# Kernel tuning notes

Measured on AMD Instinct MI355X. Metric: run time of the kernel, lower is better.

Reference implementation:

```python
import jax, jax.numpy as jnp
import numpy as np

D, H, DOUT, E, B = 1024, 4096, 1024, 8, 8192
TOP_K = 2


def setup_inputs() -> dict:
    key = jax.random.key(0)
    ks = jax.random.split(key, 12)
    s = 0.02
    return {
        "x": jax.random.normal(ks[0], (B, D), jnp.float32),
        # stacked expert params: Linear(D,H) -> ReLU -> Linear(H,H//2) -> ReLU -> Linear(H//2,DOUT)
        "W1": jax.random.normal(ks[1], (E, D, H), jnp.float32) * s,
        "b1": jnp.zeros((E, H), jnp.float32),
        "W2": jax.random.normal(ks[2], (E, H, H // 2), jnp.float32) * s,
        "b2": jnp.zeros((E, H // 2), jnp.float32),
        "W3": jax.random.normal(ks[3], (E, H // 2, DOUT), jnp.float32) * s,
        "b3": jnp.zeros((E, DOUT), jnp.float32),
        # gate: Linear(D, D//2) -> ReLU -> Linear(D//2, E) -> Softmax
        "Wg1": jax.random.normal(ks[4], (D, D // 2), jnp.float32) * s,
        "bg1": jnp.zeros((D // 2,), jnp.float32),
        "Wg2": jax.random.normal(ks[5], (D // 2, E), jnp.float32) * s,
        "bg2": jnp.zeros((E,), jnp.float32),
    }


def reference(x, W1, b1, W2, b2, W3, b3, Wg1, bg1, Wg2, bg2):
    # inference-mode math: dropout identity, no gate noise (training=False)
    num_experts = W1.shape[0]
    # gate weights: softmax over experts, [B, E]
    g = jax.nn.relu(x @ Wg1 + bg1)
    gate_weights = jax.nn.softmax(g @ Wg2 + bg2, axis=-1)
    # top-k routing, renormalized with softmax over selected logits
    top_w, top_idx = jax.lax.top_k(gate_weights, TOP_K)  # [B, k]
    top_w = jax.nn.softmax(top_w, axis=-1)
    # dense all-expert MLPs (as the original does): [E, B, *]
    h1 = jax.nn.relu(jnp.einsum("bd,edh->ebh", x, W1) + b1[:, None, :])
    h2 = jax.nn.relu(jnp.einsum("ebh,ehm->ebm", h1, W2) + b2[:, None, :])
    eo = jnp.einsum("ebm,emo->ebo", h2, W3) + b3[:, None, :]  # [E, B, DOUT]
    eo = jnp.swapaxes(eo, 0, 1)  # [B, E, DOUT]
    # gather top-k expert outputs and combine
    sel = jnp.take_along_axis(eo, top_idx[:, :, None], axis=1)  # [B, k, DOUT]
    final_output = jnp.sum(top_w[:, :, None] * sel, axis=1)  # [B, DOUT]
    # load balance loss on the (pre-topk) gate distribution
    expert_usage = jnp.mean(gate_weights, axis=0)
    load_balance_loss = jnp.mean((expert_usage - 1.0 / num_experts) ** 2)
    return final_output, load_balance_loss
```

## Files before the change

### kernel.cpp

```cpp
#include <hip/hip_runtime.h>

#define B_ROWS 8192
#define DDIM 1024
#define HDIM 4096
#define H2DIM 2048
#define DOUT_N 1024
#define NEXP 8
#define ROW_TILES 136
#define PAD_ROWS (ROW_TILES*128)

typedef __attribute__((ext_vector_type(8))) short short8;
typedef __attribute__((ext_vector_type(4))) float f32x4;

__device__ inline unsigned short f2bf(float f) {
  unsigned int u = __builtin_bit_cast(unsigned int, f);
  u += 0x7fffu + ((u >> 16) & 1u);
  return (unsigned short)(u >> 16);
}

__device__ inline void gld_lds16(const void* g, void* l) {
  __builtin_amdgcn_global_load_lds(
      (const __attribute__((address_space(1))) void*)g,
      (__attribute__((address_space(3))) void*)l, 16, 0, 0);
}

__global__ __launch_bounds__(256) void gate1_kernel(
    const float* __restrict__ x, const float* __restrict__ Wg1,
    const float* __restrict__ bg1, float* __restrict__ g) {
  __shared__ float a_s[16][132];
  __shared__ float b_s[16][64];
  const int t = threadIdx.x;
  const int row0 = blockIdx.y * 128;
  const int n0 = blockIdx.x * 64;
  const int tx = t & 15, ty = t >> 4;
  float c[8][4] = {};
  const int la_row = t >> 2, la_kq = (t & 3) * 4;
  const int lb_kk = t >> 4, lb_c = (t & 15) * 4;
  for (int k0 = 0; k0 < DDIM; k0 += 16) {
#pragma unroll
    for (int i = 0; i < 2; ++i) {
      int row = la_row + i * 64;
      float4 av = *(const float4*)&x[(size_t)(row0 + row) * DDIM + k0 + la_kq];
      a_s[la_kq + 0][row] = av.x; a_s[la_kq + 1][row] = av.y;
      a_s[la_kq + 2][row] = av.z; a_s[la_kq + 3][row] = av.w;
    }
    *(float4*)&b_s[lb_kk][lb_c] = *(const float4*)&Wg1[(size_t)(k0 + lb_kk) * 512 + n0 + lb_c];
    __syncthreads();
#pragma unroll
    for (int kk = 0; kk < 16; ++kk) {
      float4 b4 = *(const float4*)&b_s[kk][tx * 4];
      float4 a4lo = *(const float4*)&a_s[kk][ty * 8];
      float4 a4hi = *(const float4*)&a_s[kk][ty * 8 + 4];
      float aa[8] = {a4lo.x, a4lo.y, a4lo.z, a4lo.w, a4hi.x, a4hi.y, a4hi.z, a4hi.w};
      float bb[4] = {b4.x, b4.y, b4.z, b4.w};
#pragma unroll
      for (int i = 0; i < 8; ++i)
#pragma unroll
        for (int j = 0; j < 4; ++j) c[i][j] += aa[i] * bb[j];
    }
    __syncthreads();
  }
  float bb[4];
#pragma unroll
  for (int j = 0; j < 4; ++j) bb[j] = bg1[n0 + tx * 4 + j];
#pragma unroll
  for (int i = 0; i < 8; ++i) {
    float4 v;
    v.x = fmaxf(c[i][0] + bb[0], 0.f);
    v.y = fmaxf(c[i][1] + bb[1], 0.f);
    v.z = fmaxf(c[i][2] + bb[2], 0.f);
    v.w = fmaxf(c[i][3] + bb[3], 0.f);
    *(float4*)&g[(size_t)(row0 + ty * 8 + i) * 512 + n0 + tx * 4] = v;
  }
}

__global__ __launch_bounds__(256) void gate2_kernel(
    const float* __restrict__ g, const float* __restrict__ Wg2,
    const float* __restrict__ bg2, int* __restrict__ top_idx,
    float* __restrict__ top_w, int* __restrict__ counts,
    float* __restrict__ usage) {
  __shared__ float w2t[NEXP * 512];
  __shared__ float us[NEXP];
  __shared__ int cs[NEXP];
  const int t = threadIdx.x;
  for (int i = t; i < NEXP * 512; i += 256) {
    int k = i >> 3, e = i & 7;
    w2t[e * 512 + k] = Wg2[i];
  }
  if (t < NEXP) { us[t] = 0.f; cs[t] = 0; }
  __syncthreads();
  const int lane = t & 63, wid = t >> 6;
  const int row = blockIdx.x * 4 + wid;
  float part[NEXP] = {};
  const float* grow = &g[(size_t)row * 512];
#pragma unroll
  for (int j = 0; j < 8; ++j) {
    int k = lane + j * 64;
    float gv = grow[k];
#pragma unroll
    for (int e = 0; e < NEXP; ++e) part[e] += gv * w2t[e * 512 + k];
  }
#pragma unroll
  for (int e = 0; e < NEXP; ++e)
    for (int m = 32; m >= 1; m >>= 1) part[e] += __shfl_xor(part[e], m);
  if (lane == 0) {
    float p[NEXP];
    float mx = -1e30f;
#pragma unroll
    for (int e = 0; e < NEXP; ++e) { p[e] = part[e] + bg2[e]; mx = fmaxf(mx, p[e]); }
    float s = 0.f;
#pragma unroll
    for (int e = 0; e < NEXP; ++e) { p[e] = expf(p[e] - mx); s += p[e]; }
    float inv = 1.f / s;
#pragma unroll
    for (int e = 0; e < NEXP; ++e) { p[e] *= inv; atomicAdd(&us[e], p[e]); }
    int i0 = 0; float b0 = p[0];
    for (int e = 1; e < NEXP; ++e) if (p[e] > b0) { b0 = p[e]; i0 = e; }
    int i1 = -1; float b1 = -1.f;
    for (int e = 0; e < NEXP; ++e) {
      if (e == i0) continue;
      if (p[e] > b1) { b1 = p[e]; i1 = e; }
    }
    float e1 = expf(b1 - b0);
    float w0 = 1.f / (1.f + e1);
    top_idx[row * 2 + 0] = i0; top_idx[row * 2 + 1] = i1;
    top_w[row * 2 + 0] = w0;   top_w[row * 2 + 1] = e1 * w0;
    atomicAdd(&cs[i0], 1); atomicAdd(&cs[i1], 1);
  }
  __syncthreads();
  if (t < NEXP) { atomicAdd(&usage[t], us[t]); atomicAdd(&counts[t], cs[t]); }
}

__global__ void offsets_kernel(const int* __restrict__ counts, int* __restrict__ off) {
  if (threadIdx.x == 0) {
    int acc = 0;
    off[0] = 0;
    for (int e = 0; e < NEXP; ++e) {
      acc += (counts[e] + 127) & ~127;
      off[e + 1] = acc;
    }
  }
}

__global__ __launch_bounds__(256) void scatter_kernel(
    const int* __restrict__ top_idx, const int* __restrict__ off,
    int* __restrict__ fill, int* __restrict__ entry) {
  int row = blockIdx.x * 256 + threadIdx.x;
#pragma unroll
  for (int k = 0; k < 2; ++k) {
    int e = top_idx[row * 2 + k];
    int pos = atomicAdd(&fill[e], 1);
    entry[off[e] + pos] = row * 2 + k;
  }
}

__global__ __launch_bounds__(256) void gather_kernel(
    const float* __restrict__ x, const int* __restrict__ entry,
    unsigned short* __restrict__ Xg) {
  const int r = blockIdx.x;
  const int s = entry[r];
  const int t = threadIdx.x;
  unsigned long long packed = 0ull;
  if (s >= 0) {
    float4 f = *(const float4*)&x[(size_t)(s >> 1) * DDIM + t * 4];
    packed = (unsigned long long)f2bf(f.x) |
             ((unsigned long long)f2bf(f.y) << 16) |
             ((unsigned long long)f2bf(f.z) << 32) |
             ((unsigned long long)f2bf(f.w) << 48);
  }
  *(unsigned long long*)&Xg[(size_t)r * DDIM + t * 4] = packed;
}

__global__ __launch_bounds__(256) void transpose_kernel(
    const float* __restrict__ src, unsigned short* __restrict__ dst,
    int K, int N) {
  __shared__ float tile[64][65];
  const size_t eoff = (size_t)blockIdx.z * K * N;
  const int k0 = blockIdx.y * 64, n0 = blockIdx.x * 64;
  const int t = threadIdx.x;
#pragma unroll
  for (int i = 0; i < 16; ++i) {
    int idx = t + i * 256;
    int kk = idx >> 6, nn = idx & 63;
    tile[kk][nn] = src[eoff + (size_t)(k0 + kk) * N + n0 + nn];
  }
  __syncthreads();
#pragma unroll
  for (int i = 0; i < 16; ++i) {
    int idx = t + i * 256;
    int nn = idx >> 6, kk = idx & 63;
    dst[eoff + (size_t)(n0 + nn) * K + k0 + kk] = f2bf(tile[kk][nn]);
  }
}

template <int KDIM, int EPI>
__global__ __launch_bounds__(256) void expert_gemm(
    const unsigned short* __restrict__ A, const unsigned short* __restrict__ Bt,
    const float* __restrict__ bias, unsigned short* __restrict__ Cout,
    float* __restrict__ dOut, const float* __restrict__ topw,
    const int* __restrict__ entry, const int* __restrict__ off, int N) {
  const int tileM = blockIdx.y * 128;
  if (tileM >= off[NEXP]) return;
  int e = 0;
  while (e < NEXP - 1 && off[e + 1] <= tileM) ++e;
  const int tileN = blockIdx.x * 128;
  __shared__ unsigned short a_s[128 * 32];
  __shared__ unsigned short b_s[128 * 32];
  const int t = threadIdx.x;
  const int lane = t & 63, wid = t >> 6;
  const int wr = (wid & 1) * 64, wc = (wid >> 1) * 64;
  const int l16 = lane & 15, q = lane >> 4;
  f32x4 acc[4][4];
#pragma unroll
  for (int i = 0; i < 4; ++i)
#pragma unroll
    for (int j = 0; j < 4; ++j) acc[i][j] = (f32x4){0.f, 0.f, 0.f, 0.f};
  const unsigned short* Abase = A + (size_t)tileM * KDIM;
  const unsigned short* Bbase = Bt + ((size_t)e * N + tileN) * (size_t)KDIM;
  const int srow = 32 * wid;
  const int lrow = lane >> 2;
  const int lch = (lane & 3) * 8;
  for (int k0 = 0; k0 < KDIM; k0 += 32) {
#pragma unroll
    for (int j = 0; j < 2; ++j) {
      const int r0 = srow + 16 * j;
      gld_lds16(Abase + (size_t)(r0 + lrow) * KDIM + k0 + lch, &a_s[r0 * 32]);
      gld_lds16(Bbase + (size_t)(r0 + lrow) * KDIM + k0 + lch, &b_s[r0 * 32]);
    }
    __syncthreads();
    short8 af[4], bf[4];
#pragma unroll
    for (int i = 0; i < 4; ++i) {
      af[i] = *(const short8*)&a_s[(wr + 16 * i + l16) * 32 + q * 8];
      bf[i] = *(const short8*)&b_s[(wc + 16 * i + l16) * 32 + q * 8];
    }
#pragma unroll
    for (int i = 0; i < 4; ++i)
#pragma unroll
      for (int j = 0; j < 4; ++j)
        acc[i][j] = __builtin_amdgcn_mfma_f32_16x16x32_bf16(af[i], bf[j], acc[i][j], 0, 0, 0);
    __syncthreads();
  }
  if (EPI == 0) {
#pragma unroll
    for (int j = 0; j < 4; ++j) {
      const int gCol = tileN + wc + 16 * j + l16;
      const float bcol = bias[e * N + gCol];
#pragma unroll
      for (int i = 0; i < 4; ++i)
#pragma unroll
        for (int r = 0; r < 4; ++r) {
          const int gRow = tileM + wr + 16 * i + q * 4 + r;
          Cout[(size_t)gRow * N + gCol] = f2bf(fmaxf(acc[i][j][r] + bcol, 0.f));
        }
    }
  } else {
    float bcol[4];
#pragma unroll
    for (int j = 0; j < 4; ++j) bcol[j] = bias[e * N + tileN + wc + 16 * j + l16];
#pragma unroll
    for (int i = 0; i < 4; ++i)
#pragma unroll
      for (int r = 0; r < 4; ++r) {
        const int gRow = tileM + wr + 16 * i + q * 4 + r;
        const int s = entry[gRow];
        if (s < 0) continue;
        const float w = topw[s];
        float* orow = dOut + (size_t)(s >> 1) * N;
#pragma unroll
        for (int j = 0; j < 4; ++j) {
          const int gCol = tileN + wc + 16 * j + l16;
          atomicAdd(&orow[gCol], (acc[i][j][r] + bcol[j]) * w);
        }
      }
  }
}

__global__ void loss_kernel(const float* __restrict__ usage, float* __restrict__ out) {
  if (threadIdx.x == 0) {
    float l = 0.f;
    for (int e = 0; e < NEXP; ++e) {
      float d = usage[e] * (1.f / B_ROWS) - 1.f / NEXP;
      l += d * d;
    }
    out[(size_t)B_ROWS * DOUT_N] = l * (1.f / NEXP);
  }
}

extern "C" void kernel_launch(void* const* d_in, const int* in_sizes, int n_in,
                              void* d_out, int out_size, void* d_ws, size_t ws_size,
                              hipStream_t stream) {
  (void)in_sizes; (void)n_in; (void)ws_size;
  const float* x   = (const float*)d_in[0];
  const float* W1  = (const float*)d_in[1];
  const float* b1  = (const float*)d_in[2];
  const float* W2  = (const float*)d_in[3];
  const float* b2  = (const float*)d_in[4];
  const float* W3  = (const float*)d_in[5];
  const float* b3  = (const float*)d_in[6];
  const float* Wg1 = (const float*)d_in[7];
  const float* bg1 = (const float*)d_in[8];
  const float* Wg2 = (const float*)d_in[9];
  const float* bg2 = (const float*)d_in[10];
  float* out = (float*)d_out;

  char* ws = (char*)d_ws;
  size_t p = 0;
  auto alloc = [&](size_t bytes) {
    void* r = ws + p;
    p = (p + bytes + 255) & ~(size_t)255;
    return r;
  };
  int*   off    = (int*)alloc(9 * 4);
  int*   counts = (int*)alloc(NEXP * 4);
  int*   fill   = (int*)alloc(NEXP * 4);
  float* usage  = (float*)alloc(NEXP * 4);
  int*   tidx   = (int*)alloc((size_t)B_ROWS * 2 * 4);
  float* tw     = (float*)alloc((size_t)B_ROWS * 2 * 4);
  int*   entry  = (int*)alloc((size_t)PAD_ROWS * 4);
  float* g      = (float*)alloc((size_t)B_ROWS * 512 * 4);
  unsigned short* Xg  = (unsigned short*)alloc((size_t)PAD_ROWS * DDIM * 2);
  unsigned short* W1t = (unsigned short*)alloc((size_t)NEXP * HDIM * DDIM * 2);
  unsigned short* W2t = (unsigned short*)alloc((size_t)NEXP * H2DIM * HDIM * 2);
  unsigned short* W3t = (unsigned short*)alloc((size_t)NEXP * DOUT_N * H2DIM * 2);
  unsigned short* h1  = (unsigned short*)alloc((size_t)PAD_ROWS * HDIM * 2);
  unsigned short* h2  = (unsigned short*)alloc((size_t)PAD_ROWS * H2DIM * 2);

  hipMemsetAsync(d_out, 0, (size_t)out_size * 4, stream);
  hipMemsetAsync(counts, 0, NEXP * 4, stream);
  hipMemsetAsync(fill, 0, NEXP * 4, stream);
  hipMemsetAsync(usage, 0, NEXP * 4, stream);
  hipMemsetAsync(entry, 0xFF, (size_t)PAD_ROWS * 4, stream);

  transpose_kernel<<<dim3(HDIM / 64, DDIM / 64, NEXP), 256, 0, stream>>>(W1, W1t, DDIM, HDIM);
  transpose_kernel<<<dim3(H2DIM / 64, HDIM / 64, NEXP), 256, 0, stream>>>(W2, W2t, HDIM, H2DIM);
  transpose_kernel<<<dim3(DOUT_N / 64, H2DIM / 64, NEXP), 256, 0, stream>>>(W3, W3t, H2DIM, DOUT_N);

  gate1_kernel<<<dim3(512 / 64, B_ROWS / 128), 256, 0, stream>>>(x, Wg1, bg1, g);
  gate2_kernel<<<B_ROWS / 4, 256, 0, stream>>>(g, Wg2, bg2, tidx, tw, counts, usage);
  offsets_kernel<<<1, 64, 0, stream>>>(counts, off);
  scatter_kernel<<<B_ROWS / 256, 256, 0, stream>>>(tidx, off, fill, entry);
  gather_kernel<<<PAD_ROWS, 256, 0, stream>>>(x, entry, Xg);

  expert_gemm<DDIM, 0><<<dim3(HDIM / 128, ROW_TILES), 256, 0, stream>>>(
      Xg, W1t, b1, h1, nullptr, tw, entry, off, HDIM);
  expert_gemm<HDIM, 0><<<dim3(H2DIM / 128, ROW_TILES), 256, 0, stream>>>(
      h1, W2t, b2, h2, nullptr, tw, entry, off, H2DIM);
  expert_gemm<H2DIM, 1><<<dim3(DOUT_N / 128, ROW_TILES), 256, 0, stream>>>(
      h2, W3t, b3, nullptr, out, tw, entry, off, DOUT_N);

  loss_kernel<<<1, 64, 0, stream>>>(usage, out);
}
```

Measured before the change: 1.496 ms.

## Pipeline expert GEMMs with 4-stage LDS buffering, swizzle, and deterministic combine kernel

The expert GEMM moves to a 128x256 tile with 512 threads and a 4-deep LDS ring buffer filled by async global-to-LDS loads. It waits with explicit vmcnt counts and raw barriers instead of a full sync per K step, XOR-swizzles LDS columns to avoid bank conflicts, remaps workgroups across XCDs, and raises MFMA priority. The last GEMM no longer issues per-element atomicAdd into the output. It writes expert outputs to a buffer that reuses h1, and a new combine kernel applies the top-2 weights using positions recorded by scatter. This removes atomic traffic and sync stalls, at the cost of higher LDS use per block and an extra kernel pass over the expert outputs.

```diff
diff --git a/kernel.cpp b/kernel.cpp
--- a/kernel.cpp
+++ b/kernel.cpp
@@ -22,6 +22,14 @@
   __builtin_amdgcn_global_load_lds(
       (const __attribute__((address_space(1))) void*)g,
       (__attribute__((address_space(3))) void*)l, 16, 0, 0);
+}
+
+#define WAITV(N) asm volatile("s_waitcnt vmcnt(" #N ")" ::: "memory")
+
+__device__ inline void barrier_raw() {
+  asm volatile("" ::: "memory");
+  __builtin_amdgcn_s_barrier();
+  asm volatile("" ::: "memory");
 }
 
 __global__ __launch_bounds__(256) void gate1_kernel(
@@ -144,13 +152,14 @@
 
 __global__ __launch_bounds__(256) void scatter_kernel(
     const int* __restrict__ top_idx, const int* __restrict__ off,
-    int* __restrict__ fill, int* __restrict__ entry) {
+    int* __restrict__ fill, int* __restrict__ entry, int* __restrict__ posof) {
   int row = blockIdx.x * 256 + threadIdx.x;
 #pragma unroll
   for (int k = 0; k < 2; ++k) {
     int e = top_idx[row * 2 + k];
     int pos = atomicAdd(&fill[e], 1);
     entry[off[e] + pos] = row * 2 + k;
+    posof[row * 2 + k] = off[e] + pos;
   }
 }
 
@@ -194,86 +203,167 @@
 }
 
 template <int KDIM, int EPI>
-__global__ __launch_bounds__(256) void expert_gemm(
+__global__ __launch_bounds__(512, 2) void expert_gemm(
     const unsigned short* __restrict__ A, const unsigned short* __restrict__ Bt,
     const float* __restrict__ bias, unsigned short* __restrict__ Cout,
-    float* __restrict__ dOut, const float* __restrict__ topw,
-    const int* __restrict__ entry, const int* __restrict__ off, int N) {
-  const int tileM = blockIdx.y * 128;
+    float* __restrict__ Eo, const int* __restrict__ off, int N) {
+  constexpr int NS = KDIM / 32;
+  static_assert(NS >= 4, "need >=4 K sub-tiles");
+  __shared__ unsigned short smem[4 * 12288];
+
+  const int gx = gridDim.x;
+  const int nwg = gx * gridDim.y;
+  const int orig = blockIdx.x + gx * blockIdx.y;
+  const int cpx = nwg >> 3;
+  const int swz = (orig & 7) * cpx + (orig >> 3);
+  const int tm = swz / gx, tn = swz - tm * gx;
+  const int tileM = tm * 128;
   if (tileM >= off[NEXP]) return;
   int e = 0;
   while (e < NEXP - 1 && off[e + 1] <= tileM) ++e;
-  const int tileN = blockIdx.x * 128;
-  __shared__ unsigned short a_s[128 * 32];
-  __shared__ unsigned short b_s[128 * 32];
+  const int tileN = tn * 256;
+
   const int t = threadIdx.x;
   const int lane = t & 63, wid = t >> 6;
-  const int wr = (wid & 1) * 64, wc = (wid >> 1) * 64;
+  const int wr = (wid >> 2) * 64;
+  const int wc = (wid & 3) * 64;
   const int l16 = lane & 15, q = lane >> 4;
-  f32x4 acc[4][4];
-#pragma unroll
-  for (int i = 0; i < 4; ++i)
-#pragma unroll
-    for (int j = 0; j < 4; ++j) acc[i][j] = (f32x4){0.f, 0.f, 0.f, 0.f};
+
   const unsigned short* Abase = A + (size_t)tileM * KDIM;
   const unsigned short* Bbase = Bt + ((size_t)e * N + tileN) * (size_t)KDIM;
-  const int srow = 32 * wid;
-  const int lrow = lane >> 2;
-  const int lch = (lane & 3) * 8;
-  for (int k0 = 0; k0 < KDIM; k0 += 32) {
+
+  const int srow0 = wid * 16 + (lane >> 2);
+  const int scp = lane & 3;
+
+  f32x4 acc[4][4];
+#pragma unroll
+  for (int i = 0; i < 4; ++i)
+#pragma unroll
+    for (int j = 0; j < 4; ++j) acc[i][j] = (f32x4){0.f, 0.f, 0.f, 0.f};
+
+  auto stage = [&](int s) {
+    unsigned short* buf = &smem[(size_t)(s & 3) * 12288];
+    const int k0 = s * 32;
+    {
+      const int row = srow0;
+      const int c = scp ^ ((row >> 1) & 3);
+      gld_lds16(Abase + (size_t)row * KDIM + k0 + c * 8,
+                buf + (size_t)(wid * 16) * 32);
+    }
 #pragma unroll
     for (int j = 0; j < 2; ++j) {
-      const int r0 = srow + 16 * j;
-      gld_lds16(Abase + (size_t)(r0 + lrow) * KDIM + k0 + lch, &a_s[r0 * 32]);
-      gld_lds16(Bbase + (size_t)(r0 + lrow) * KDIM + k0 + lch, &b_s[r0 * 32]);
-    }
-    __syncthreads();
-    short8 af[4], bf[4];
+      const int row = j * 128 + srow0;
+      const int c = scp ^ ((row >> 1) & 3);
+      gld_lds16(Bbase + (size_t)row * KDIM + k0 + c * 8,
+                buf + 4096 + (size_t)(j * 128 + wid * 16) * 32);
+    }
+  };
+
+  auto rdfrags = [&](int s, short8* af, short8* bf) {
+    const unsigned short* buf = &smem[(size_t)(s & 3) * 12288];
 #pragma unroll
     for (int i = 0; i < 4; ++i) {
-      af[i] = *(const short8*)&a_s[(wr + 16 * i + l16) * 32 + q * 8];
-      bf[i] = *(const short8*)&b_s[(wc + 16 * i + l16) * 32 + q * 8];
-    }
+      const int row = wr + 16 * i + l16;
+      const int c = q ^ ((row >> 1) & 3);
+      af[i] = *(const short8*)&buf[row * 32 + c * 8];
+    }
+#pragma unroll
+    for (int j = 0; j < 4; ++j) {
+      const int row = wc + 16 * j + l16;
+      const int c = q ^ ((row >> 1) & 3);
+      bf[j] = *(const short8*)&buf[4096 + row * 32 + c * 8];
+    }
+  };
+
+  auto domfma = [&](short8* af, short8* bf) {
+    __builtin_amdgcn_s_setprio(1);
 #pragma unroll
     for (int i = 0; i < 4; ++i)
 #pragma unroll
       for (int j = 0; j < 4; ++j)
         acc[i][j] = __builtin_amdgcn_mfma_f32_16x16x32_bf16(af[i], bf[j], acc[i][j], 0, 0, 0);
-    __syncthreads();
-  }
+    __builtin_amdgcn_s_setprio(0);
+  };
+
+  stage(0); stage(1); stage(2);
+  WAITV(6);
+  barrier_raw();
+
+#pragma unroll 4
+  for (int s = 0; s < NS - 3; ++s) {
+    short8 af[4], bf[4];
+    rdfrags(s, af, bf);
+    stage(s + 3);
+    domfma(af, bf);
+    WAITV(6);
+    barrier_raw();
+  }
+  {
+    short8 af[4], bf[4];
+    rdfrags(NS - 3, af, bf);
+    domfma(af, bf);
+    WAITV(3);
+    barrier_raw();
+  }
+  {
+    short8 af[4], bf[4];
+    rdfrags(NS - 2, af, bf);
+    domfma(af, bf);
+    WAITV(0);
+    barrier_raw();
+  }
+  {
+    short8 af[4], bf[4];
+    rdfrags(NS - 1, af, bf);
+    domfma(af, bf);
+  }
+
   if (EPI == 0) {
 #pragma unroll
     for (int j = 0; j < 4; ++j) {
       const int gCol = tileN + wc + 16 * j + l16;
       const float bcol = bias[e * N + gCol];
 #pragma unroll
-      for (int i = 0; i < 4; ++i)
-#pragma unroll
-        for (int r = 0; r < 4; ++r) {
-          const int gRow = tileM + wr + 16 * i + q * 4 + r;
-          Cout[(size_t)gRow * N + gCol] = f2bf(fmaxf(acc[i][j][r] + bcol, 0.f));
-        }
+      for (int i = 0; i < 4; ++i) {
+        const int gRow0 = tileM + wr + 16 * i + q * 4;
+#pragma unroll
+        for (int r = 0; r < 4; ++r)
+          Cout[(size_t)(gRow0 + r) * N + gCol] = f2bf(fmaxf(acc[i][j][r] + bcol, 0.f));
+      }
     }
   } else {
     float bcol[4];
 #pragma unroll
     for (int j = 0; j < 4; ++j) bcol[j] = bias[e * N + tileN + wc + 16 * j + l16];
 #pragma unroll
-    for (int i = 0; i < 4; ++i)
+    for (int i = 0; i < 4; ++i) {
+      const int gRow0 = tileM + wr + 16 * i + q * 4;
 #pragma unroll
       for (int r = 0; r < 4; ++r) {
-        const int gRow = tileM + wr + 16 * i + q * 4 + r;
-        const int s = entry[gRow];
-        if (s < 0) continue;
-        const float w = topw[s];
-        float* orow = dOut + (size_t)(s >> 1) * N;
-#pragma unroll
-        for (int j = 0; j < 4; ++j) {
-          const int gCol = tileN + wc + 16 * j + l16;
-          atomicAdd(&orow[gCol], (acc[i][j][r] + bcol[j]) * w);
-        }
+        float* orow = Eo + (size_t)(gRow0 + r) * N;
+#pragma unroll
+        for (int j = 0; j < 4; ++j)
+          orow[tileN + wc + 16 * j + l16] = acc[i][j][r] + bcol[j];
       }
-  }
+    }
+  }
+}
+
+__global__ __launch_bounds__(256) void combine_kernel(
+    const float* __restrict__ eo, const int* __restrict__ posof,
+    const float* __restrict__ tw, float* __restrict__ out) {
+  const int row = blockIdx.x;
+  const int c = threadIdx.x * 4;
+  const int p0 = posof[row * 2 + 0], p1 = posof[row * 2 + 1];
+  const float w0 = tw[row * 2 + 0], w1 = tw[row * 2 + 1];
+  float4 a = *(const float4*)&eo[(size_t)p0 * DOUT_N + c];
+  float4 b = *(const float4*)&eo[(size_t)p1 * DOUT_N + c];
+  float4 o;
+  o.x = w0 * a.x + w1 * b.x;
+  o.y = w0 * a.y + w1 * b.y;
+  o.z = w0 * a.z + w1 * b.z;
+  o.w = w0 * a.w + w1 * b.w;
+  *(float4*)&out[(size_t)row * DOUT_N + c] = o;
 }
 
 __global__ void loss_kernel(const float* __restrict__ usage, float* __restrict__ out) {
@@ -317,6 +407,7 @@
   float* usage  = (float*)alloc(NEXP * 4);
   int*   tidx   = (int*)alloc((size_t)B_ROWS * 2 * 4);
   float* tw     = (float*)alloc((size_t)B_ROWS * 2 * 4);
+  int*   posof  = (int*)alloc((size_t)B_ROWS * 2 * 4);
   int*   entry  = (int*)alloc((size_t)PAD_ROWS * 4);
   float* g      = (float*)alloc((size_t)B_ROWS * 512 * 4);
   unsigned short* Xg  = (unsigned short*)alloc((size_t)PAD_ROWS * DDIM * 2);
@@ -325,6 +416,7 @@
   unsigned short* W3t = (unsigned short*)alloc((size_t)NEXP * DOUT_N * H2DIM * 2);
   unsigned short* h1  = (unsigned short*)alloc((size_t)PAD_ROWS * HDIM * 2);
   unsigned short* h2  = (unsigned short*)alloc((size_t)PAD_ROWS * H2DIM * 2);
+  float* eo = (float*)h1;
 
   hipMemsetAsync(d_out, 0, (size_t)out_size * 4, stream);
   hipMemsetAsync(counts, 0, NEXP * 4, stream);
@@ -339,15 +431,16 @@
   gate1_kernel<<<dim3(512 / 64, B_ROWS / 128), 256, 0, stream>>>(x, Wg1, bg1, g);
   gate2_kernel<<<B_ROWS / 4, 256, 0, stream>>>(g, Wg2, bg2, tidx, tw, counts, usage);
   offsets_kernel<<<1, 64, 0, stream>>>(counts, off);
-  scatter_kernel<<<B_ROWS / 256, 256, 0, stream>>>(tidx, off, fill, entry);
+  scatter_kernel<<<B_ROWS / 256, 256, 0, stream>>>(tidx, off, fill, entry, posof);
   gather_kernel<<<PAD_ROWS, 256, 0, stream>>>(x, entry, Xg);
 
-  expert_gemm<DDIM, 0><<<dim3(HDIM / 128, ROW_TILES), 256, 0, stream>>>(
-      Xg, W1t, b1, h1, nullptr, tw, entry, off, HDIM);
-  expert_gemm<HDIM, 0><<<dim3(H2DIM / 128, ROW_TILES), 256, 0, stream>>>(
-      h1, W2t, b2, h2, nullptr, tw, entry, off, H2DIM);
-  expert_gemm<H2DIM, 1><<<dim3(DOUT_N / 128, ROW_TILES), 256, 0, stream>>>(
-      h2, W3t, b3, nullptr, out, tw, entry, off, DOUT_N);
+  expert_gemm<DDIM, 0><<<dim3(HDIM / 256, ROW_TILES), 512, 0, stream>>>(
+      Xg, W1t, b1, h1, nullptr, off, HDIM);
+  expert_gemm<HDIM, 0><<<dim3(H2DIM / 256, ROW_TILES), 512, 0, stream>>>(
+      h1, W2t, b2, h2, nullptr, off, H2DIM);
+  expert_gemm<H2DIM, 1><<<dim3(DOUT_N / 256, ROW_TILES), 512, 0, stream>>>(
+      h2, W3t, b3, nullptr, eo, off, DOUT_N);
+  combine_kernel<<<B_ROWS, 256, 0, stream>>>(eo, posof, tw, out);
 
   loss_kernel<<<1, 64, 0, stream>>>(usage, out);
 }
```

Measured after the change: 1.492 ms. About the same (-0.3%).
